# Optimization experiments

Measured on AMD Instinct MI355X. Metric: run time of the kernel, lower is better.

The kernel has to match this reference:

```python
import jax, jax.numpy as jnp
import numpy as np
from jax import lax

DN = ('NCHW', 'OIHW', 'NCHW')

def conv(x, w, pad='VALID'):
    return lax.conv_general_dilated(x, w, (1, 1), pad, dimension_numbers=DN)

def adaptive_matrix(in_s, out_s):
    # exact torch adaptive_avg_pool2d bin weights: start=floor(i*in/out), end=ceil((i+1)*in/out)
    M = np.zeros((out_s, in_s), np.float32)
    for i in range(out_s):
        s = (i * in_s) // out_s
        e = -(-((i + 1) * in_s) // out_s)
        M[i, s:e] = 1.0 / (e - s)
    return jnp.asarray(M)

def setup_inputs() -> dict:
    key = jax.random.key(0)
    ks = jax.random.split(key, 11)
    C = 64
    def w(k, shape, fan_in):
        return jax.random.normal(k, shape, jnp.float32) * (1.0 / np.sqrt(fan_in))
    return {
        'x': jax.random.normal(ks[0], (16, C, 128, 128), jnp.float32),
        'conv1_w': w(ks[1], (2 * C, C, 1, 1), C),
        'conv1_b': jnp.zeros((2 * C,), jnp.float32),
        'conv2_w': w(ks[2], (C, C, 1, 1), C),
        'conv2_b': jnp.zeros((C,), jnp.float32),
        'conv3_w': w(ks[3], (C, 2 * C, 1, 1), 2 * C),
        'conv3_b': jnp.zeros((C,), jnp.float32),
        'pos_w': w(ks[4], (C, C, 3, 3), C * 9),
        'pos_b': jnp.zeros((C,), jnp.float32),
        'se_w1': w(ks[5], (C // 8, C, 1, 1), C),
        'se_w2': w(ks[6], (C, C // 8, 1, 1), C // 8),
    }

def reference(x, conv1_w, conv1_b, conv2_w, conv2_b, conv3_w, conv3_b, pos_w, pos_b, se_w1, se_w2):
    C, nw, ext = 64, 4, 4
    y = conv(x, conv1_w) + conv1_b[None, :, None, None]
    x1, x2 = y[:, :C], y[:, C:]
    N, _, H, W = x1.shape
    x1p = jnp.pad(x1, ((0, 0), (0, 0), (ext, ext), (ext, ext)), mode='edge')
    Hp, Wp = H + 2 * ext, W + 2 * ext
    Hs, Ws = H // nw, W // nw
    Hk, Wk = Hs + H % nw, Ws + W % nw
    Hps, Wps = Hp // nw, Wp // nw
    Hpk, Wpk = Hps + Hp % nw, Wps + Wp % nw
    # unfold: windows row-major (h_window fastest over j), shape (N, nw^2, C, Hpk, Wpk)
    wins = jnp.stack([x1p[:, :, i * Hps:i * Hps + Hpk, j * Wps:j * Wps + Wpk]
                      for i in range(nw) for j in range(nw)], axis=1)
    Ph = adaptive_matrix(Hpk, Hk)
    Pw = adaptive_matrix(Wpk, Wk)
    pooled = jnp.einsum('nlchw,Hh,Ww->nlcHW', wins, Ph, Pw).reshape(N * nw * nw, C, Hk, Wk)
    pr = (conv(pooled, conv2_w) + conv2_b[None, :, None, None]
          + conv(pooled, pos_w, 'SAME') + pos_b[None, :, None, None])
    # SE attention
    s = jnp.mean(pr, axis=(2, 3), keepdims=True)
    s = jax.nn.sigmoid(conv(jax.nn.relu(conv(s, se_w1)), se_w2))
    att = pr * s + pr
    # faithful torch .view(N, C*Hk*Wk, nw^2) memory reinterpretation, then fold
    cols = att.reshape(N, nw * nw * C * Hk * Wk).reshape(N, C, Hk, Wk, nw * nw)
    out = jnp.zeros((N, C, H, W), x.dtype)
    cnt = jnp.zeros((N, 1, H, W), x.dtype)
    for i in range(nw):
        for j in range(nw):
            l = i * nw + j
            out = out.at[:, :, i * Hs:i * Hs + Hk, j * Ws:j * Ws + Wk].add(cols[..., l])
            cnt = cnt.at[:, :, i * Hs:i * Hs + Hk, j * Ws:j * Ws + Wk].add(1.0)
    out = out / cnt
    return conv(jnp.concatenate([out, x2], axis=1), conv3_w) + conv3_b[None, :, None, None]
```

## Files before the change

kernel.cpp:

```cpp
#include <hip/hip_runtime.h>

constexpr int N = 16, C = 64, H = 128, W = 128, P = H * W;
constexpr int NL = 256, PK = 1024;

constexpr size_t OFF_RA    = 0;
constexpr size_t OFF_RB    = 8388608;
constexpr size_t OFF_RC    = 16777216;
constexpr size_t OFF_SUMS  = 33554432;
constexpr size_t OFF_SCALE = OFF_SUMS  + 16384;
constexpr size_t OFF_WMOD  = OFF_SCALE + 16384;
constexpr size_t OFF_W1L   = OFF_WMOD  + 18432;
constexpr size_t OFF_W3L   = OFF_W1L   + 4096;

typedef short bf16x8 __attribute__((ext_vector_type(8)));
typedef float f32x4  __attribute__((ext_vector_type(4)));

__device__ inline unsigned short f2bf(float f) {
    unsigned u = __float_as_uint(f);
    unsigned r = (u + 0x7FFFu + ((u >> 16) & 1u)) >> 16;
    return (unsigned short)r;
}
__device__ inline float bf2f(unsigned short h) {
    return __uint_as_float(((unsigned)h) << 16);
}

__global__ __launch_bounds__(256) void k0_prep(const float* __restrict__ pos_w,
                                               const float* __restrict__ conv2_w,
                                               const float* __restrict__ w1,
                                               const float* __restrict__ w3,
                                               unsigned short* __restrict__ wmod,
                                               unsigned short* __restrict__ w1lay,
                                               unsigned short* __restrict__ w3lay,
                                               float* __restrict__ sums) {
    int t = blockIdx.x * 256 + threadIdx.x;
    if (t < 36864) {
        int cir = t & 31;
        int co  = (t >> 5) & 63;
        int cib = (t >> 11) & 1;
        int tap = t >> 12;
        int ci  = cib * 32 + cir;
        float v = pos_w[(co * 64 + ci) * 9 + tap];
        if (tap == 4) v += conv2_w[co * 64 + ci];
        wmod[t] = f2bf(v);
    } else if (t < 45056) {
        int u = t - 36864;
        int cir = u & 31;
        int co  = (u >> 5) & 127;
        int cib = u >> 12;
        w1lay[u] = f2bf(w1[co * 64 + cib * 32 + cir]);
    } else if (t < 53248) {
        int u = t - 45056;
        int cir = u & 31;
        int co  = (u >> 5) & 63;
        int cib = u >> 11;
        w3lay[u] = f2bf(w3[co * 128 + cib * 32 + cir]);
    } else {
        sums[t - 53248] = 0.f;
    }
}

__global__ __launch_bounds__(256) void k1_conv1(const float* __restrict__ x,
                                                const unsigned short* __restrict__ w1lay,
                                                const float* __restrict__ b1,
                                                unsigned short* __restrict__ x1t,
                                                unsigned short* __restrict__ x2t) {
    __shared__ __align__(16) float lda[64 * 65];
    __shared__ __align__(16) unsigned short ldb[128 * 64];
    int bid = blockIdx.x;
    int n   = bid >> 7;
    int px0 = (bid & 127) << 7;
    int t   = threadIdx.x;
    #pragma unroll
    for (int s = 0; s < 2; ++s) {
        if (s) __syncthreads();
        const float* src = x + (size_t)n * 64 * P + px0 + s * 64;
        #pragma unroll
        for (int k = 0; k < 4; ++k) {
            int u = t + k * 256;
            int ci = u >> 4, px4 = u & 15;
            float4 v = *(const float4*)(src + (size_t)ci * P + px4 * 4);
            float* d = lda + ci * 65 + px4 * 4;
            d[0] = v.x; d[1] = v.y; d[2] = v.z; d[3] = v.w;
        }
        __syncthreads();
        int cig = t & 15, pxl = t >> 4;
        #pragma unroll
        for (int k = 0; k < 4; ++k) {
            int px = pxl + k * 16;
            ushort4 o;
            o.x = f2bf(lda[(cig * 4 + 0) * 65 + px]);
            o.y = f2bf(lda[(cig * 4 + 1) * 65 + px]);
            o.z = f2bf(lda[(cig * 4 + 2) * 65 + px]);
            o.w = f2bf(lda[(cig * 4 + 3) * 65 + px]);
            int pg = s * 64 + px;
            int chunk = cig >> 1;
            *(ushort4*)(ldb + pg * 64 + ((chunk ^ (pg & 7)) * 8) + (cig & 1) * 4) = o;
        }
    }
    __syncthreads();
    int wave = t >> 6, lane = t & 63;
    int quad = lane >> 4, l16 = lane & 15;
    int pxw = wave * 32;
    f32x4 acc[8][2] = {};
    #pragma unroll
    for (int cib = 0; cib < 2; ++cib) {
        bf16x8 af[8], bfr[2];
        #pragma unroll
        for (int ct = 0; ct < 8; ++ct)
            af[ct] = *(const bf16x8*)(w1lay + ((size_t)(cib * 128 + ct * 16 + l16)) * 32 + quad * 8);
        #pragma unroll
        for (int pt = 0; pt < 2; ++pt) {
            int pg = pxw + pt * 16 + l16;
            int chunk = cib * 4 + quad;
            bfr[pt] = *(const bf16x8*)(ldb + pg * 64 + ((chunk ^ (pg & 7)) * 8));
        }
        #pragma unroll
        for (int ct = 0; ct < 8; ++ct)
            #pragma unroll
            for (int pt = 0; pt < 2; ++pt)
                acc[ct][pt] = __builtin_amdgcn_mfma_f32_16x16x32_bf16(af[ct], bfr[pt], acc[ct][pt], 0, 0, 0);
    }
    #pragma unroll
    for (int ct = 0; ct < 8; ++ct) {
        int co0 = ct * 16 + quad * 4;
        float4 bb = *(const float4*)(b1 + co0);
        #pragma unroll
        for (int pt = 0; pt < 2; ++pt) {
            int px = px0 + pxw + pt * 16 + l16;
            ushort4 o;
            o.x = f2bf(acc[ct][pt][0] + bb.x);
            o.y = f2bf(acc[ct][pt][1] + bb.y);
            o.z = f2bf(acc[ct][pt][2] + bb.z);
            o.w = f2bf(acc[ct][pt][3] + bb.w);
            if (co0 < 64)
                *(ushort4*)(x1t + ((size_t)n * P + px) * 64 + co0) = o;
            else
                *(ushort4*)(x2t + ((size_t)n * P + px) * 64 + (co0 - 64)) = o;
        }
    }
}

__global__ __launch_bounds__(256) void k3_pool_pr(const unsigned short* __restrict__ x1t,
                                                  const unsigned short* __restrict__ wmod,
                                                  const float* __restrict__ b2,
                                                  const float* __restrict__ posb,
                                                  unsigned short* __restrict__ prb,
                                                  float* __restrict__ sums) {
    __shared__ __align__(16) unsigned short lxs[340 * 32];
    int bid = blockIdx.x;
    int nl  = bid >> 2;
    int r0  = (bid & 3) * 8;
    int n   = nl >> 4, wl = nl & 15;
    int wi  = wl >> 2, wj = wl & 3;
    int t   = threadIdx.x;
    const unsigned short* xb = x1t + (size_t)n * P * 64;
    int wave = t >> 6, lane = t & 63;
    int quad = lane >> 4, l16 = lane & 15;
    int wrow0 = wave * 2;
    f32x4 acc[4][4] = {};
    #pragma unroll
    for (int cib = 0; cib < 2; ++cib) {
        if (cib) __syncthreads();
        for (int it = 0; it < 6; ++it) {
            int e = t + it * 256;
            if (e < 1360) {
                int pix = e >> 2, part = e & 3;
                int lr = pix / 34, lc = pix - lr * 34;
                int gr = r0 - 1 + lr, gc = lc - 1;
                unsigned short oc[8];
                if ((unsigned)gr < 32u && (unsigned)gc < 32u) {
                    int sh = gr + (gr >> 4), sw = gc + (gc >> 4);
                    int u = wi * 34 + sh - 4, v = wj * 34 + sw - 4;
                    int ra = min(max(u, 0), 127), rb = min(max(u + 1, 0), 127);
                    int ca = min(max(v, 0), 127), cb = min(max(v + 1, 0), 127);
                    int off = cib * 32 + part * 8;
                    uint4 A = *(const uint4*)(xb + (size_t)(ra * 128 + ca) * 64 + off);
                    uint4 B = *(const uint4*)(xb + (size_t)(ra * 128 + cb) * 64 + off);
                    uint4 Cc = *(const uint4*)(xb + (size_t)(rb * 128 + ca) * 64 + off);
                    uint4 D = *(const uint4*)(xb + (size_t)(rb * 128 + cb) * 64 + off);
                    const unsigned short* a = (const unsigned short*)&A;
                    const unsigned short* b = (const unsigned short*)&B;
                    const unsigned short* c = (const unsigned short*)&Cc;
                    const unsigned short* d = (const unsigned short*)&D;
                    #pragma unroll
                    for (int q = 0; q < 8; ++q)
                        oc[q] = f2bf(0.25f * (bf2f(a[q]) + bf2f(b[q]) + bf2f(c[q]) + bf2f(d[q])));
                } else {
                    #pragma unroll
                    for (int q = 0; q < 8; ++q) oc[q] = 0;
                }
                *(uint4*)(lxs + pix * 32 + ((part ^ ((pix >> 1) & 3)) * 8)) = *(const uint4*)oc;
            }
        }
        __syncthreads();
        #pragma unroll
        for (int tap = 0; tap < 9; ++tap) {
            int dh = tap / 3, dw = tap % 3;
            bf16x8 af[4], bfr[4];
            #pragma unroll
            for (int ct = 0; ct < 4; ++ct)
                af[ct] = *(const bf16x8*)(wmod + (((tap * 2 + cib) * 64) + ct * 16 + l16) * 32 + quad * 8);
            #pragma unroll
            for (int pt = 0; pt < 4; ++pt) {
                int pix = (wrow0 + (pt >> 1) + dh) * 34 + ((pt & 1) * 16 + l16 + dw);
                bfr[pt] = *(const bf16x8*)(lxs + pix * 32 + ((quad ^ ((pix >> 1) & 3)) * 8));
            }
            #pragma unroll
            for (int ct = 0; ct < 4; ++ct)
                #pragma unroll
                for (int pt = 0; pt < 4; ++pt)
                    acc[ct][pt] = __builtin_amdgcn_mfma_f32_16x16x32_bf16(af[ct], bfr[pt], acc[ct][pt], 0, 0, 0);
        }
    }
    #pragma unroll
    for (int ct = 0; ct < 4; ++ct) {
        #pragma unroll
        for (int r = 0; r < 4; ++r) {
            int co = ct * 16 + quad * 4 + r;
            float bias = b2[co] + posb[co];
            float s = 0.f;
            #pragma unroll
            for (int pt = 0; pt < 4; ++pt) {
                float v = acc[ct][pt][r] + bias;
                int row = r0 + wrow0 + (pt >> 1);
                int col = (pt & 1) * 16 + l16;
                prb[(size_t)nl * 65536 + co * 1024 + row * 32 + col] = f2bf(v);
                s += v;
            }
            s += __shfl_xor(s, 1);
            s += __shfl_xor(s, 2);
            s += __shfl_xor(s, 4);
            s += __shfl_xor(s, 8);
            if (l16 == 0) atomicAdd(&sums[nl * 64 + co], s);
        }
    }
}

__global__ __launch_bounds__(64) void k3b_se(const float* __restrict__ sums,
                                             const float* __restrict__ w1,
                                             const float* __restrict__ w2,
                                             float* __restrict__ scale) {
    __shared__ float m[64];
    __shared__ float hid[8];
    int nl = blockIdx.x;
    int t  = threadIdx.x;
    m[t] = sums[nl * 64 + t] * (1.f / 1024.f);
    __syncthreads();
    if (t < 8) {
        float s = 0.f;
        #pragma unroll
        for (int ci = 0; ci < 64; ++ci) s += w1[t * 64 + ci] * m[ci];
        hid[t] = fmaxf(s, 0.f);
    }
    __syncthreads();
    float v = 0.f;
    #pragma unroll
    for (int r = 0; r < 8; ++r) v += w2[t * 8 + r] * hid[r];
    scale[nl * 64 + t] = 1.f + 1.f / (1.f + __expf(-v));
}

__global__ __launch_bounds__(256) void k5_conv3(const unsigned short* __restrict__ prb,
                                                const float* __restrict__ scale,
                                                const unsigned short* __restrict__ x2t,
                                                const unsigned short* __restrict__ w3lay,
                                                const float* __restrict__ b3,
                                                float* __restrict__ out) {
    __shared__ __align__(16) unsigned short lxs[128 * 136];
    int bid = blockIdx.x;
    int n   = bid >> 7;
    int row = bid & 127;
    int i   = row >> 5, h2 = row & 31;
    int px0 = row << 7;
    int t   = threadIdx.x;
    const unsigned short* src2 = x2t + ((size_t)n * P + (size_t)row * 128) * 64;
    #pragma unroll
    for (int it = 0; it < 4; ++it) {
        int e = t + it * 256;
        int pix = e >> 3, part = e & 7;
        *(uint4*)(lxs + pix * 136 + 64 + part * 8) = *(const uint4*)(src2 + pix * 64 + part * 8);
    }
    int c2 = t >> 5, w2 = t & 31;
    int cc_b = h2 >> 1;
    int hb = (h2 & 1) * 512 + w2 * 16 + i * 4;
    #pragma unroll
    for (int mm = 0; mm < 2; ++mm) {
        int nl = n * 16 + c2 * 2 + mm;
        const unsigned short* pb = prb + (size_t)nl * 65536 + (size_t)cc_b * 1024 + hb;
        const float* sb = scale + nl * 64 + cc_b;
        ushort4 v0 = *(const ushort4*)(pb);
        ushort4 v1 = *(const ushort4*)(pb + 16 * 1024);
        ushort4 v2 = *(const ushort4*)(pb + 32 * 1024);
        ushort4 v3 = *(const ushort4*)(pb + 48 * 1024);
        float s0 = sb[0], s1 = sb[16], s2 = sb[32], s3 = sb[48];
        unsigned short* d = lxs + w2 * 136 + c2 * 8 + mm * 4;
        ushort4 o;
        o.x = f2bf(bf2f(v0.x) * s0); o.y = f2bf(bf2f(v1.x) * s1);
        o.z = f2bf(bf2f(v2.x) * s2); o.w = f2bf(bf2f(v3.x) * s3);
        *(ushort4*)(d) = o;
        o.x = f2bf(bf2f(v0.y) * s0); o.y = f2bf(bf2f(v1.y) * s1);
        o.z = f2bf(bf2f(v2.y) * s2); o.w = f2bf(bf2f(v3.y) * s3);
        *(ushort4*)(d + 32 * 136) = o;
        o.x = f2bf(bf2f(v0.z) * s0); o.y = f2bf(bf2f(v1.z) * s1);
        o.z = f2bf(bf2f(v2.z) * s2); o.w = f2bf(bf2f(v3.z) * s3);
        *(ushort4*)(d + 64 * 136) = o;
        o.x = f2bf(bf2f(v0.w) * s0); o.y = f2bf(bf2f(v1.w) * s1);
        o.z = f2bf(bf2f(v2.w) * s2); o.w = f2bf(bf2f(v3.w) * s3);
        *(ushort4*)(d + 96 * 136) = o;
    }
    __syncthreads();
    int wave = t >> 6, lane = t & 63;
    int quad = lane >> 4, l16 = lane & 15;
    int pxw = wave * 32;
    f32x4 acc[4][2] = {};
    #pragma unroll
    for (int cib = 0; cib < 4; ++cib) {
        bf16x8 af[4], bfr[2];
        #pragma unroll
        for (int ct = 0; ct < 4; ++ct)
            af[ct] = *(const bf16x8*)(w3lay + ((size_t)(cib * 64 + ct * 16 + l16)) * 32 + quad * 8);
        #pragma unroll
        for (int pt = 0; pt < 2; ++pt)
            bfr[pt] = *(const bf16x8*)(lxs + (pxw + pt * 16 + l16) * 136 + cib * 32 + quad * 8);
        #pragma unroll
        for (int ct = 0; ct < 4; ++ct)
            #pragma unroll
            for (int pt = 0; pt < 2; ++pt)
                acc[ct][pt] = __builtin_amdgcn_mfma_f32_16x16x32_bf16(af[ct], bfr[pt], acc[ct][pt], 0, 0, 0);
    }
    #pragma unroll
    for (int ct = 0; ct < 4; ++ct) {
        int co0 = ct * 16 + quad * 4;
        float4 bb = *(const float4*)(b3 + co0);
        #pragma unroll
        for (int pt = 0; pt < 2; ++pt) {
            int px = px0 + pxw + pt * 16 + l16;
            const float* bp = (const float*)&bb;
            #pragma unroll
            for (int r = 0; r < 4; ++r)
                out[((size_t)n * 64 + co0 + r) * P + px] = acc[ct][pt][r] + bp[r];
        }
    }
}

extern "C" void kernel_launch(void* const* d_in, const int* in_sizes, int n_in,
                              void* d_out, int out_size, void* d_ws, size_t ws_size,
                              hipStream_t stream) {
    const float* x       = (const float*)d_in[0];
    const float* conv1_w = (const float*)d_in[1];
    const float* conv1_b = (const float*)d_in[2];
    const float* conv2_w = (const float*)d_in[3];
    const float* conv2_b = (const float*)d_in[4];
    const float* conv3_w = (const float*)d_in[5];
    const float* conv3_b = (const float*)d_in[6];
    const float* pos_w   = (const float*)d_in[7];
    const float* pos_b   = (const float*)d_in[8];
    const float* se_w1   = (const float*)d_in[9];
    const float* se_w2   = (const float*)d_in[10];

    float* ws = (float*)d_ws;
    unsigned short* prb  = (unsigned short*)(ws + OFF_RA);
    unsigned short* x1t  = (unsigned short*)(ws + OFF_RB);
    unsigned short* x2t  = (unsigned short*)(ws + OFF_RC);
    float* sums  = ws + OFF_SUMS;
    float* scale = ws + OFF_SCALE;
    unsigned short* wmod  = (unsigned short*)(ws + OFF_WMOD);
    unsigned short* w1lay = (unsigned short*)(ws + OFF_W1L);
    unsigned short* w3lay = (unsigned short*)(ws + OFF_W3L);

    k0_prep      <<<272,  256, 0, stream>>>(pos_w, conv2_w, conv1_w, conv3_w,
                                            wmod, w1lay, w3lay, sums);
    k1_conv1     <<<2048, 256, 0, stream>>>(x, w1lay, conv1_b, x1t, x2t);
    k3_pool_pr   <<<1024, 256, 0, stream>>>(x1t, wmod, conv2_b, pos_b, prb, sums);
    k3b_se       <<<256,  64,  0, stream>>>(sums, se_w1, se_w2, scale);
    k5_conv3     <<<2048, 256, 0, stream>>>(prb, scale, x2t, w3lay, conv3_b, (float*)d_out);
}
```

Before: 238.7 us.

## Split pooling into its own kernel, shrink conv tiles, load conv1 inputs directly

Pooling moves out of the 3x3-conv kernel into a new k2_pool kernel. That kernel writes a padded, swizzled bf16 pooled tensor to workspace once, so the conv kernel no longer recomputes halo rows and just copies tiles into LDS. The conv kernel now uses 4-row tiles over twice as many blocks. conv1 drops its LDS transpose and has each lane gather its bf16 operands straight from global memory with strided scalar loads. The cost is an extra launch, an extra round trip of the pooled tensor through memory, and uncoalesced loads in conv1. The workspace layout is also changed so x1t and prb alias.

```diff
diff --git a/kernel.cpp b/kernel.cpp
--- a/kernel.cpp
+++ b/kernel.cpp
@@ -3,10 +3,10 @@
 constexpr int N = 16, C = 64, H = 128, W = 128, P = H * W;
 constexpr int NL = 256, PK = 1024;
 
-constexpr size_t OFF_RA    = 0;
-constexpr size_t OFF_RB    = 8388608;
-constexpr size_t OFF_RC    = 16777216;
-constexpr size_t OFF_SUMS  = 33554432;
+constexpr size_t OFF_A     = 0;
+constexpr size_t OFF_POOL  = 8388608;
+constexpr size_t OFF_X2    = 17858560;
+constexpr size_t OFF_SUMS  = 26247168;
 constexpr size_t OFF_SCALE = OFF_SUMS  + 16384;
 constexpr size_t OFF_WMOD  = OFF_SCALE + 16384;
 constexpr size_t OFF_W1L   = OFF_WMOD  + 18432;
@@ -64,61 +64,38 @@
                                                 const float* __restrict__ b1,
                                                 unsigned short* __restrict__ x1t,
                                                 unsigned short* __restrict__ x2t) {
-    __shared__ __align__(16) float lda[64 * 65];
-    __shared__ __align__(16) unsigned short ldb[128 * 64];
     int bid = blockIdx.x;
     int n   = bid >> 7;
     int px0 = (bid & 127) << 7;
     int t   = threadIdx.x;
-    #pragma unroll
-    for (int s = 0; s < 2; ++s) {
-        if (s) __syncthreads();
-        const float* src = x + (size_t)n * 64 * P + px0 + s * 64;
-        #pragma unroll
-        for (int k = 0; k < 4; ++k) {
-            int u = t + k * 256;
-            int ci = u >> 4, px4 = u & 15;
-            float4 v = *(const float4*)(src + (size_t)ci * P + px4 * 4);
-            float* d = lda + ci * 65 + px4 * 4;
-            d[0] = v.x; d[1] = v.y; d[2] = v.z; d[3] = v.w;
-        }
-        __syncthreads();
-        int cig = t & 15, pxl = t >> 4;
-        #pragma unroll
-        for (int k = 0; k < 4; ++k) {
-            int px = pxl + k * 16;
-            ushort4 o;
-            o.x = f2bf(lda[(cig * 4 + 0) * 65 + px]);
-            o.y = f2bf(lda[(cig * 4 + 1) * 65 + px]);
-            o.z = f2bf(lda[(cig * 4 + 2) * 65 + px]);
-            o.w = f2bf(lda[(cig * 4 + 3) * 65 + px]);
-            int pg = s * 64 + px;
-            int chunk = cig >> 1;
-            *(ushort4*)(ldb + pg * 64 + ((chunk ^ (pg & 7)) * 8) + (cig & 1) * 4) = o;
-        }
-    }
-    __syncthreads();
     int wave = t >> 6, lane = t & 63;
     int quad = lane >> 4, l16 = lane & 15;
     int pxw = wave * 32;
+    const float* xb = x + (size_t)n * 64 * P + px0 + pxw + l16;
+    bf16x8 bfr[2][2];
+    #pragma unroll
+    for (int cib = 0; cib < 2; ++cib) {
+        #pragma unroll
+        for (int pt = 0; pt < 2; ++pt) {
+            unsigned short tmp[8];
+            #pragma unroll
+            for (int q = 0; q < 8; ++q)
+                tmp[q] = f2bf(xb[(size_t)(cib * 32 + quad * 8 + q) * P + pt * 16]);
+            bfr[cib][pt] = *(const bf16x8*)tmp;
+        }
+    }
     f32x4 acc[8][2] = {};
     #pragma unroll
     for (int cib = 0; cib < 2; ++cib) {
-        bf16x8 af[8], bfr[2];
+        bf16x8 af[8];
         #pragma unroll
         for (int ct = 0; ct < 8; ++ct)
             af[ct] = *(const bf16x8*)(w1lay + ((size_t)(cib * 128 + ct * 16 + l16)) * 32 + quad * 8);
         #pragma unroll
-        for (int pt = 0; pt < 2; ++pt) {
-            int pg = pxw + pt * 16 + l16;
-            int chunk = cib * 4 + quad;
-            bfr[pt] = *(const bf16x8*)(ldb + pg * 64 + ((chunk ^ (pg & 7)) * 8));
-        }
-        #pragma unroll
         for (int ct = 0; ct < 8; ++ct)
             #pragma unroll
             for (int pt = 0; pt < 2; ++pt)
-                acc[ct][pt] = __builtin_amdgcn_mfma_f32_16x16x32_bf16(af[ct], bfr[pt], acc[ct][pt], 0, 0, 0);
+                acc[ct][pt] = __builtin_amdgcn_mfma_f32_16x16x32_bf16(af[ct], bfr[cib][pt], acc[ct][pt], 0, 0, 0);
     }
     #pragma unroll
     for (int ct = 0; ct < 8; ++ct) {
@@ -140,75 +117,94 @@
     }
 }
 
-__global__ __launch_bounds__(256) void k3_pool_pr(const unsigned short* __restrict__ x1t,
-                                                  const unsigned short* __restrict__ wmod,
-                                                  const float* __restrict__ b2,
-                                                  const float* __restrict__ posb,
-                                                  unsigned short* __restrict__ prb,
-                                                  float* __restrict__ sums) {
-    __shared__ __align__(16) unsigned short lxs[340 * 32];
+__global__ __launch_bounds__(256) void k2_pool(const unsigned short* __restrict__ x1t,
+                                               unsigned short* __restrict__ pooled) {
+    int tg = blockIdx.x * 256 + threadIdx.x;
+    int nlcib = tg / 1156;
+    int pix   = tg - nlcib * 1156;
+    int nl = nlcib >> 1, cib = nlcib & 1;
+    int n = nl >> 4, wl = nl & 15;
+    int wi = wl >> 2, wj = wl & 3;
+    int pr = pix / 34, pc = pix - pr * 34;
+    int gr = pr - 1, gc = pc - 1;
+    unsigned short oc[32];
+    if ((unsigned)gr < 32u && (unsigned)gc < 32u) {
+        int sh = gr + (gr >> 4), sw = gc + (gc >> 4);
+        int u = wi * 34 + sh - 4, v = wj * 34 + sw - 4;
+        int ra = min(max(u, 0), 127), rb = min(max(u + 1, 0), 127);
+        int ca = min(max(v, 0), 127), cb = min(max(v + 1, 0), 127);
+        const unsigned short* xb = x1t + (size_t)n * P * 64 + cib * 32;
+        const unsigned short* pA = xb + (size_t)(ra * 128 + ca) * 64;
+        const unsigned short* pB = xb + (size_t)(ra * 128 + cb) * 64;
+        const unsigned short* pC = xb + (size_t)(rb * 128 + ca) * 64;
+        const unsigned short* pD = xb + (size_t)(rb * 128 + cb) * 64;
+        #pragma unroll
+        for (int h = 0; h < 4; ++h) {
+            uint4 A  = *(const uint4*)(pA + h * 8);
+            uint4 B  = *(const uint4*)(pB + h * 8);
+            uint4 Cc = *(const uint4*)(pC + h * 8);
+            uint4 D  = *(const uint4*)(pD + h * 8);
+            const unsigned short* a = (const unsigned short*)&A;
+            const unsigned short* b = (const unsigned short*)&B;
+            const unsigned short* c = (const unsigned short*)&Cc;
+            const unsigned short* d = (const unsigned short*)&D;
+            #pragma unroll
+            for (int q = 0; q < 8; ++q)
+                oc[h * 8 + q] = f2bf(0.25f * (bf2f(a[q]) + bf2f(b[q]) + bf2f(c[q]) + bf2f(d[q])));
+        }
+    } else {
+        #pragma unroll
+        for (int q = 0; q < 32; ++q) oc[q] = 0;
+    }
+    unsigned short* dst = pooled + ((size_t)nlcib * 1156 + pix) * 32;
+    int sx = (pix >> 1) & 3;
+    #pragma unroll
+    for (int p = 0; p < 4; ++p)
+        *(uint4*)(dst + ((p ^ sx) * 8)) = *(const uint4*)(oc + p * 8);
+}
+
+__global__ __launch_bounds__(256) void k3_conv(const unsigned short* __restrict__ pooled,
+                                               const unsigned short* __restrict__ wmod,
+                                               const float* __restrict__ b2,
+                                               const float* __restrict__ posb,
+                                               unsigned short* __restrict__ prb,
+                                               float* __restrict__ sums) {
+    __shared__ __align__(16) unsigned short lxs[204 * 32];
     int bid = blockIdx.x;
-    int nl  = bid >> 2;
-    int r0  = (bid & 3) * 8;
-    int n   = nl >> 4, wl = nl & 15;
-    int wi  = wl >> 2, wj = wl & 3;
+    int nl  = bid >> 3;
+    int r0  = (bid & 7) * 4;
     int t   = threadIdx.x;
-    const unsigned short* xb = x1t + (size_t)n * P * 64;
     int wave = t >> 6, lane = t & 63;
     int quad = lane >> 4, l16 = lane & 15;
-    int wrow0 = wave * 2;
-    f32x4 acc[4][4] = {};
+    int wrow0 = wave;
+    f32x4 acc[4][2] = {};
     #pragma unroll
     for (int cib = 0; cib < 2; ++cib) {
         if (cib) __syncthreads();
-        for (int it = 0; it < 6; ++it) {
+        const unsigned short* src = pooled + ((size_t)(nl * 2 + cib) * 1156 + r0 * 34) * 32;
+        #pragma unroll
+        for (int it = 0; it < 4; ++it) {
             int e = t + it * 256;
-            if (e < 1360) {
-                int pix = e >> 2, part = e & 3;
-                int lr = pix / 34, lc = pix - lr * 34;
-                int gr = r0 - 1 + lr, gc = lc - 1;
-                unsigned short oc[8];
-                if ((unsigned)gr < 32u && (unsigned)gc < 32u) {
-                    int sh = gr + (gr >> 4), sw = gc + (gc >> 4);
-                    int u = wi * 34 + sh - 4, v = wj * 34 + sw - 4;
-                    int ra = min(max(u, 0), 127), rb = min(max(u + 1, 0), 127);
-                    int ca = min(max(v, 0), 127), cb = min(max(v + 1, 0), 127);
-                    int off = cib * 32 + part * 8;
-                    uint4 A = *(const uint4*)(xb + (size_t)(ra * 128 + ca) * 64 + off);
-                    uint4 B = *(const uint4*)(xb + (size_t)(ra * 128 + cb) * 64 + off);
-                    uint4 Cc = *(const uint4*)(xb + (size_t)(rb * 128 + ca) * 64 + off);
-                    uint4 D = *(const uint4*)(xb + (size_t)(rb * 128 + cb) * 64 + off);
-                    const unsigned short* a = (const unsigned short*)&A;
-                    const unsigned short* b = (const unsigned short*)&B;
-                    const unsigned short* c = (const unsigned short*)&Cc;
-                    const unsigned short* d = (const unsigned short*)&D;
-                    #pragma unroll
-                    for (int q = 0; q < 8; ++q)
-                        oc[q] = f2bf(0.25f * (bf2f(a[q]) + bf2f(b[q]) + bf2f(c[q]) + bf2f(d[q])));
-                } else {
-                    #pragma unroll
-                    for (int q = 0; q < 8; ++q) oc[q] = 0;
-                }
-                *(uint4*)(lxs + pix * 32 + ((part ^ ((pix >> 1) & 3)) * 8)) = *(const uint4*)oc;
-            }
+            if (e < 816)
+                *(uint4*)(lxs + e * 8) = *(const uint4*)(src + e * 8);
         }
         __syncthreads();
         #pragma unroll
         for (int tap = 0; tap < 9; ++tap) {
             int dh = tap / 3, dw = tap % 3;
-            bf16x8 af[4], bfr[4];
+            bf16x8 af[4], bfr[2];
             #pragma unroll
             for (int ct = 0; ct < 4; ++ct)
                 af[ct] = *(const bf16x8*)(wmod + (((tap * 2 + cib) * 64) + ct * 16 + l16) * 32 + quad * 8);
             #pragma unroll
-            for (int pt = 0; pt < 4; ++pt) {
-                int pix = (wrow0 + (pt >> 1) + dh) * 34 + ((pt & 1) * 16 + l16 + dw);
+            for (int pt = 0; pt < 2; ++pt) {
+                int pix = (wrow0 + dh) * 34 + (pt * 16 + l16 + dw);
                 bfr[pt] = *(const bf16x8*)(lxs + pix * 32 + ((quad ^ ((pix >> 1) & 3)) * 8));
             }
             #pragma unroll
             for (int ct = 0; ct < 4; ++ct)
                 #pragma unroll
-                for (int pt = 0; pt < 4; ++pt)
+                for (int pt = 0; pt < 2; ++pt)
                     acc[ct][pt] = __builtin_amdgcn_mfma_f32_16x16x32_bf16(af[ct], bfr[pt], acc[ct][pt], 0, 0, 0);
         }
     }
@@ -220,10 +216,10 @@
             float bias = b2[co] + posb[co];
             float s = 0.f;
             #pragma unroll
-            for (int pt = 0; pt < 4; ++pt) {
+            for (int pt = 0; pt < 2; ++pt) {
                 float v = acc[ct][pt][r] + bias;
-                int row = r0 + wrow0 + (pt >> 1);
-                int col = (pt & 1) * 16 + l16;
+                int row = r0 + wrow0;
+                int col = pt * 16 + l16;
                 prb[(size_t)nl * 65536 + co * 1024 + row * 32 + col] = f2bf(v);
                 s += v;
             }
@@ -358,19 +354,21 @@
     const float* se_w2   = (const float*)d_in[10];
 
     float* ws = (float*)d_ws;
-    unsigned short* prb  = (unsigned short*)(ws + OFF_RA);
-    unsigned short* x1t  = (unsigned short*)(ws + OFF_RB);
-    unsigned short* x2t  = (unsigned short*)(ws + OFF_RC);
+    unsigned short* x1t    = (unsigned short*)(ws + OFF_A);
+    unsigned short* prb    = (unsigned short*)(ws + OFF_A);
+    unsigned short* pooled = (unsigned short*)(ws + OFF_POOL);
+    unsigned short* x2t    = (unsigned short*)(ws + OFF_X2);
     float* sums  = ws + OFF_SUMS;
     float* scale = ws + OFF_SCALE;
     unsigned short* wmod  = (unsigned short*)(ws + OFF_WMOD);
     unsigned short* w1lay = (unsigned short*)(ws + OFF_W1L);
     unsigned short* w3lay = (unsigned short*)(ws + OFF_W3L);
 
-    k0_prep      <<<272,  256, 0, stream>>>(pos_w, conv2_w, conv1_w, conv3_w,
-                                            wmod, w1lay, w3lay, sums);
-    k1_conv1     <<<2048, 256, 0, stream>>>(x, w1lay, conv1_b, x1t, x2t);
-    k3_pool_pr   <<<1024, 256, 0, stream>>>(x1t, wmod, conv2_b, pos_b, prb, sums);
-    k3b_se       <<<256,  64,  0, stream>>>(sums, se_w1, se_w2, scale);
-    k5_conv3     <<<2048, 256, 0, stream>>>(prb, scale, x2t, w3lay, conv3_b, (float*)d_out);
-}
+    k0_prep  <<<272,  256, 0, stream>>>(pos_w, conv2_w, conv1_w, conv3_w,
+                                        wmod, w1lay, w3lay, sums);
+    k1_conv1 <<<2048, 256, 0, stream>>>(x, w1lay, conv1_b, x1t, x2t);
+    k2_pool  <<<2312, 256, 0, stream>>>(x1t, pooled);
+    k3_conv  <<<2048, 256, 0, stream>>>(pooled, wmod, conv2_b, pos_b, prb, sums);
+    k3b_se   <<<256,  64,  0, stream>>>(sums, se_w1, se_w2, scale);
+    k5_conv3 <<<2048, 256, 0, stream>>>(prb, scale, x2t, w3lay, conv3_b, (float*)d_out);
+}
```

Result: slower. 280.0 us (+17.3%).

## Load conv1 input straight into MFMA fragments and stage all pool channels once

Applied to the files above, without the earlier changes.

In conv1, the LDS transpose staging and its barriers are removed. Each lane now reads its eight channel values directly from global memory with strided scalar loads and packs them into bf16 fragments. In the pool/conv kernel, all 64 channels of the pooled tile are staged into a doubled LDS buffer in one pass with a new swizzle, which drops the second staging pass and barrier. The workspace sums offset is also moved down. The trade-offs are less coalesced global loads in conv1 and larger shared memory per block in the pool kernel, which may lower occupancy.

```diff
diff --git a/kernel.cpp b/kernel.cpp
--- a/kernel.cpp
+++ b/kernel.cpp
@@ -6,7 +6,7 @@
 constexpr size_t OFF_RA    = 0;
 constexpr size_t OFF_RB    = 8388608;
 constexpr size_t OFF_RC    = 16777216;
-constexpr size_t OFF_SUMS  = 33554432;
+constexpr size_t OFF_SUMS  = 25165824;
 constexpr size_t OFF_SCALE = OFF_SUMS  + 16384;
 constexpr size_t OFF_WMOD  = OFF_SCALE + 16384;
 constexpr size_t OFF_W1L   = OFF_WMOD  + 18432;
@@ -64,61 +64,38 @@
                                                 const float* __restrict__ b1,
                                                 unsigned short* __restrict__ x1t,
                                                 unsigned short* __restrict__ x2t) {
-    __shared__ __align__(16) float lda[64 * 65];
-    __shared__ __align__(16) unsigned short ldb[128 * 64];
     int bid = blockIdx.x;
     int n   = bid >> 7;
     int px0 = (bid & 127) << 7;
     int t   = threadIdx.x;
-    #pragma unroll
-    for (int s = 0; s < 2; ++s) {
-        if (s) __syncthreads();
-        const float* src = x + (size_t)n * 64 * P + px0 + s * 64;
-        #pragma unroll
-        for (int k = 0; k < 4; ++k) {
-            int u = t + k * 256;
-            int ci = u >> 4, px4 = u & 15;
-            float4 v = *(const float4*)(src + (size_t)ci * P + px4 * 4);
-            float* d = lda + ci * 65 + px4 * 4;
-            d[0] = v.x; d[1] = v.y; d[2] = v.z; d[3] = v.w;
-        }
-        __syncthreads();
-        int cig = t & 15, pxl = t >> 4;
-        #pragma unroll
-        for (int k = 0; k < 4; ++k) {
-            int px = pxl + k * 16;
-            ushort4 o;
-            o.x = f2bf(lda[(cig * 4 + 0) * 65 + px]);
-            o.y = f2bf(lda[(cig * 4 + 1) * 65 + px]);
-            o.z = f2bf(lda[(cig * 4 + 2) * 65 + px]);
-            o.w = f2bf(lda[(cig * 4 + 3) * 65 + px]);
-            int pg = s * 64 + px;
-            int chunk = cig >> 1;
-            *(ushort4*)(ldb + pg * 64 + ((chunk ^ (pg & 7)) * 8) + (cig & 1) * 4) = o;
-        }
-    }
-    __syncthreads();
     int wave = t >> 6, lane = t & 63;
     int quad = lane >> 4, l16 = lane & 15;
     int pxw = wave * 32;
+    const float* xb = x + (size_t)n * 64 * P + px0 + pxw + l16;
+    bf16x8 bfr[2][2];
+    #pragma unroll
+    for (int cib = 0; cib < 2; ++cib) {
+        #pragma unroll
+        for (int pt = 0; pt < 2; ++pt) {
+            unsigned short tmp[8];
+            #pragma unroll
+            for (int q = 0; q < 8; ++q)
+                tmp[q] = f2bf(xb[(size_t)(cib * 32 + quad * 8 + q) * P + pt * 16]);
+            bfr[cib][pt] = *(const bf16x8*)tmp;
+        }
+    }
     f32x4 acc[8][2] = {};
     #pragma unroll
     for (int cib = 0; cib < 2; ++cib) {
-        bf16x8 af[8], bfr[2];
+        bf16x8 af[8];
         #pragma unroll
         for (int ct = 0; ct < 8; ++ct)
             af[ct] = *(const bf16x8*)(w1lay + ((size_t)(cib * 128 + ct * 16 + l16)) * 32 + quad * 8);
         #pragma unroll
-        for (int pt = 0; pt < 2; ++pt) {
-            int pg = pxw + pt * 16 + l16;
-            int chunk = cib * 4 + quad;
-            bfr[pt] = *(const bf16x8*)(ldb + pg * 64 + ((chunk ^ (pg & 7)) * 8));
-        }
-        #pragma unroll
         for (int ct = 0; ct < 8; ++ct)
             #pragma unroll
             for (int pt = 0; pt < 2; ++pt)
-                acc[ct][pt] = __builtin_amdgcn_mfma_f32_16x16x32_bf16(af[ct], bfr[pt], acc[ct][pt], 0, 0, 0);
+                acc[ct][pt] = __builtin_amdgcn_mfma_f32_16x16x32_bf16(af[ct], bfr[cib][pt], acc[ct][pt], 0, 0, 0);
     }
     #pragma unroll
     for (int ct = 0; ct < 8; ++ct) {
@@ -146,7 +123,7 @@
                                                   const float* __restrict__ posb,
                                                   unsigned short* __restrict__ prb,
                                                   float* __restrict__ sums) {
-    __shared__ __align__(16) unsigned short lxs[340 * 32];
+    __shared__ __align__(16) unsigned short lxs[340 * 64];
     int bid = blockIdx.x;
     int nl  = bid >> 2;
     int r0  = (bid & 3) * 8;
@@ -154,45 +131,44 @@
     int wi  = wl >> 2, wj = wl & 3;
     int t   = threadIdx.x;
     const unsigned short* xb = x1t + (size_t)n * P * 64;
+    for (int it = 0; it < 11; ++it) {
+        int e = t + it * 256;
+        if (e < 2720) {
+            int pix = e >> 3, part = e & 7;
+            int lr = pix / 34, lc = pix - lr * 34;
+            int gr = r0 - 1 + lr, gc = lc - 1;
+            unsigned short oc[8];
+            if ((unsigned)gr < 32u && (unsigned)gc < 32u) {
+                int sh = gr + (gr >> 4), sw = gc + (gc >> 4);
+                int u = wi * 34 + sh - 4, v = wj * 34 + sw - 4;
+                int ra = min(max(u, 0), 127), rb = min(max(u + 1, 0), 127);
+                int ca = min(max(v, 0), 127), cb = min(max(v + 1, 0), 127);
+                int off = part * 8;
+                uint4 A = *(const uint4*)(xb + (size_t)(ra * 128 + ca) * 64 + off);
+                uint4 B = *(const uint4*)(xb + (size_t)(ra * 128 + cb) * 64 + off);
+                uint4 Cc = *(const uint4*)(xb + (size_t)(rb * 128 + ca) * 64 + off);
+                uint4 D = *(const uint4*)(xb + (size_t)(rb * 128 + cb) * 64 + off);
+                const unsigned short* a = (const unsigned short*)&A;
+                const unsigned short* b = (const unsigned short*)&B;
+                const unsigned short* c = (const unsigned short*)&Cc;
+                const unsigned short* d = (const unsigned short*)&D;
+                #pragma unroll
+                for (int q = 0; q < 8; ++q)
+                    oc[q] = f2bf(0.25f * (bf2f(a[q]) + bf2f(b[q]) + bf2f(c[q]) + bf2f(d[q])));
+            } else {
+                #pragma unroll
+                for (int q = 0; q < 8; ++q) oc[q] = 0;
+            }
+            *(uint4*)(lxs + pix * 64 + ((part ^ (pix & 7)) * 8)) = *(const uint4*)oc;
+        }
+    }
+    __syncthreads();
     int wave = t >> 6, lane = t & 63;
     int quad = lane >> 4, l16 = lane & 15;
     int wrow0 = wave * 2;
     f32x4 acc[4][4] = {};
     #pragma unroll
     for (int cib = 0; cib < 2; ++cib) {
-        if (cib) __syncthreads();
-        for (int it = 0; it < 6; ++it) {
-            int e = t + it * 256;
-            if (e < 1360) {
-                int pix = e >> 2, part = e & 3;
-                int lr = pix / 34, lc = pix - lr * 34;
-                int gr = r0 - 1 + lr, gc = lc - 1;
-                unsigned short oc[8];
-                if ((unsigned)gr < 32u && (unsigned)gc < 32u) {
-                    int sh = gr + (gr >> 4), sw = gc + (gc >> 4);
-                    int u = wi * 34 + sh - 4, v = wj * 34 + sw - 4;
-                    int ra = min(max(u, 0), 127), rb = min(max(u + 1, 0), 127);
-                    int ca = min(max(v, 0), 127), cb = min(max(v + 1, 0), 127);
-                    int off = cib * 32 + part * 8;
-                    uint4 A = *(const uint4*)(xb + (size_t)(ra * 128 + ca) * 64 + off);
-                    uint4 B = *(const uint4*)(xb + (size_t)(ra * 128 + cb) * 64 + off);
-                    uint4 Cc = *(const uint4*)(xb + (size_t)(rb * 128 + ca) * 64 + off);
-                    uint4 D = *(const uint4*)(xb + (size_t)(rb * 128 + cb) * 64 + off);
-                    const unsigned short* a = (const unsigned short*)&A;
-                    const unsigned short* b = (const unsigned short*)&B;
-                    const unsigned short* c = (const unsigned short*)&Cc;
-                    const unsigned short* d = (const unsigned short*)&D;
-                    #pragma unroll
-                    for (int q = 0; q < 8; ++q)
-                        oc[q] = f2bf(0.25f * (bf2f(a[q]) + bf2f(b[q]) + bf2f(c[q]) + bf2f(d[q])));
-                } else {
-                    #pragma unroll
-                    for (int q = 0; q < 8; ++q) oc[q] = 0;
-                }
-                *(uint4*)(lxs + pix * 32 + ((part ^ ((pix >> 1) & 3)) * 8)) = *(const uint4*)oc;
-            }
-        }
-        __syncthreads();
         #pragma unroll
         for (int tap = 0; tap < 9; ++tap) {
             int dh = tap / 3, dw = tap % 3;
@@ -203,7 +179,8 @@
             #pragma unroll
             for (int pt = 0; pt < 4; ++pt) {
                 int pix = (wrow0 + (pt >> 1) + dh) * 34 + ((pt & 1) * 16 + l16 + dw);
-                bfr[pt] = *(const bf16x8*)(lxs + pix * 32 + ((quad ^ ((pix >> 1) & 3)) * 8));
+                int chunk = cib * 4 + quad;
+                bfr[pt] = *(const bf16x8*)(lxs + pix * 64 + ((chunk ^ (pix & 7)) * 8));
             }
             #pragma unroll
             for (int ct = 0; ct < 4; ++ct)
@@ -367,10 +344,10 @@
     unsigned short* w1lay = (unsigned short*)(ws + OFF_W1L);
     unsigned short* w3lay = (unsigned short*)(ws + OFF_W3L);
 
-    k0_prep      <<<272,  256, 0, stream>>>(pos_w, conv2_w, conv1_w, conv3_w,
-                                            wmod, w1lay, w3lay, sums);
-    k1_conv1     <<<2048, 256, 0, stream>>>(x, w1lay, conv1_b, x1t, x2t);
-    k3_pool_pr   <<<1024, 256, 0, stream>>>(x1t, wmod, conv2_b, pos_b, prb, sums);
-    k3b_se       <<<256,  64,  0, stream>>>(sums, se_w1, se_w2, scale);
-    k5_conv3     <<<2048, 256, 0, stream>>>(prb, scale, x2t, w3lay, conv3_b, (float*)d_out);
-}
+    k0_prep   <<<272,  256, 0, stream>>>(pos_w, conv2_w, conv1_w, conv3_w,
+                                         wmod, w1lay, w3lay, sums);
+    k1_conv1  <<<2048, 256, 0, stream>>>(x, w1lay, conv1_b, x1t, x2t);
+    k3_pool_pr<<<1024, 256, 0, stream>>>(x1t, wmod, conv2_b, pos_b, prb, sums);
+    k3b_se    <<<256,  64,  0, stream>>>(sums, se_w1, se_w2, scale);
+    k5_conv3  <<<2048, 256, 0, stream>>>(prb, scale, x2t, w3lay, conv3_b, (float*)d_out);
+}
```

Result: no change. 235.5 us (-1.3%).
